# Kernel optimization log

Measured on AMD Instinct MI355X. Metric: run time of the kernel, lower is better.

Reference implementation:

```python
import jax, jax.numpy as jnp
import numpy as np

N_LAYERS = 2  # config['layer']
U_, L_, T_, A_ = 200000, 20000, 48, 2000
D_, D3_ = 96, 32
NNZ_ = 2_000_000


def _spmm(rows, cols, vals, x, n_rows):
    # y = A @ x for COO sparse A of shape [n_rows, n_cols]; x: [n_cols, d]
    return jax.ops.segment_sum(vals[:, None] * x[cols], rows, num_segments=n_rows)


def _attn_fuse(z, W1, b1, w2):
    # Attention module: project = Linear(d3,d3)+Tanh+Linear(d3,1, no bias)
    # z: [N, C, d3]; softmax over the C fused channels (dim=1)
    w = jnp.tanh(z @ W1 + b1) @ w2            # [N, C, 1]
    beta = jax.nn.softmax(w, axis=1)
    return jnp.sum(beta * z, axis=1)          # [N, d3]


def setup_inputs() -> dict:
    key = jax.random.key(0)
    ks = iter(jax.random.split(key, 64))
    inp = {}
    inp['user_emb'] = jax.random.normal(next(ks), (U_, D_), jnp.float32) * 0.1
    inp['loc_emb'] = jax.random.normal(next(ks), (L_, D3_), jnp.float32) * 0.1
    inp['time_emb'] = jax.random.normal(next(ks), (T_, D3_), jnp.float32) * 0.1
    inp['act_emb'] = jax.random.normal(next(ks), (A_, D3_), jnp.float32) * 0.1
    for f in ('l', 't', 'a'):
        s = 1.0 / np.sqrt(D3_)
        inp[f'W1_{f}'] = jax.random.normal(next(ks), (D3_, D3_), jnp.float32) * s
        inp[f'b1_{f}'] = jnp.zeros((D3_,), jnp.float32)
        inp[f'w2_{f}'] = jax.random.normal(next(ks), (D3_, 1), jnp.float32) * s

    def add_sparse(prefix, n_rows, n_cols):
        inp[prefix + '_rows'] = jax.random.randint(next(ks), (NNZ_,), 0, n_rows, jnp.int32)
        inp[prefix + '_cols'] = jax.random.randint(next(ks), (NNZ_,), 0, n_cols, jnp.int32)
        inp[prefix + '_vals'] = jax.random.uniform(next(ks), (NNZ_,), jnp.float32) * 0.01

    for p in ('normL', 'normT', 'normA', 'normLT', 'normLA', 'normTA', 'normLTA'):
        add_sparse(p, U_, U_)
    add_sparse('vtoeL', L_, U_)
    add_sparse('vtoeT', T_, U_)
    add_sparse('vtoeA', A_, U_)
    return inp


def reference(user_emb, loc_emb, time_emb, act_emb,
              W1_l, b1_l, w2_l, W1_t, b1_t, w2_t, W1_a, b1_a, w2_a,
              normL_rows, normL_cols, normL_vals,
              normT_rows, normT_cols, normT_vals,
              normA_rows, normA_cols, normA_vals,
              normLT_rows, normLT_cols, normLT_vals,
              normLA_rows, normLA_cols, normLA_vals,
              normTA_rows, normTA_cols, normTA_vals,
              normLTA_rows, normLTA_cols, normLTA_vals,
              vtoeL_rows, vtoeL_cols, vtoeL_vals,
              vtoeT_rows, vtoeT_cols, vtoeT_vals,
              vtoeA_rows, vtoeA_cols, vtoeA_vals):
    U = user_emb.shape[0]
    L, T, A = loc_emb.shape[0], time_emb.shape[0], act_emb.shape[0]
    # disentangle user embedding into 3 factor chunks (torch.split)
    u_l, u_t, u_a = jnp.split(user_emb, 3, axis=-1)
    u_l_all, u_t_all, u_a_all = [u_l], [u_t], [u_a]
    l_e, t_e, a_e = loc_emb, time_emb, act_emb
    l_all, t_all, a_all = [l_e], [t_e], [a_e]
    for _ in range(N_LAYERS):
        # intra-type hypergraph propagation per factor (4 hyperedge types each)
        zl = jnp.stack([
            _spmm(normL_rows, normL_cols, normL_vals, u_l, U),
            _spmm(normLT_rows, normLT_cols, normLT_vals, u_l, U),
            _spmm(normLA_rows, normLA_cols, normLA_vals, u_l, U),
            _spmm(normLTA_rows, normLTA_cols, normLTA_vals, u_l, U)], axis=1)
        zt = jnp.stack([
            _spmm(normT_rows, normT_cols, normT_vals, u_t, U),
            _spmm(normLT_rows, normLT_cols, normLT_vals, u_t, U),
            _spmm(normTA_rows, normTA_cols, normTA_vals, u_t, U),
            _spmm(normLTA_rows, normLTA_cols, normLTA_vals, u_t, U)], axis=1)
        za = jnp.stack([
            _spmm(normA_rows, normA_cols, normA_vals, u_a, U),
            _spmm(normLA_rows, normLA_cols, normLA_vals, u_a, U),
            _spmm(normTA_rows, normTA_cols, normTA_vals, u_a, U),
            _spmm(normLTA_rows, normLTA_cols, normLTA_vals, u_a, U)], axis=1)
        # hyperedge (location/time/activity) updates: vertex -> edge aggregation
        l_e = _spmm(vtoeL_rows, vtoeL_cols, vtoeL_vals, u_l, L)
        t_e = _spmm(vtoeT_rows, vtoeT_cols, vtoeT_vals, u_t, T)
        a_e = _spmm(vtoeA_rows, vtoeA_cols, vtoeA_vals, u_a, A)
        # inter-type attention fusion
        u_l = _attn_fuse(zl, W1_l, b1_l, w2_l)
        u_t = _attn_fuse(zt, W1_t, b1_t, w2_t)
        u_a = _attn_fuse(za, W1_a, b1_a, w2_a)
        u_l_all.append(u_l); u_t_all.append(u_t); u_a_all.append(u_a)
        l_all.append(l_e); t_all.append(t_e); a_all.append(a_e)
    mean = lambda xs: jnp.mean(jnp.stack(xs, 0), 0)
    users = jnp.concatenate([mean(u_l_all), mean(u_t_all), mean(u_a_all)], axis=-1)
    return users, mean(l_all), mean(t_all), mean(a_all)
```

## Files before the change

kernel.cpp:

```cpp
#include <hip/hip_runtime.h>
#include <cmath>

#define U_N 200000
#define L_N 20000
#define T_N 48
#define A_N 2000

#define VAL_SCALE_INV 9.5367431640625e-7f
#define BSHIFT 6
#define CAP_U 800
#define NBUCK_U 3125
#define CHUNK 8192
#define NSL_SH 3
#define NSL (1 << NSL_SH)
#define CAP_SL 40
#define NSA_SH 5
#define NSA (1 << NSA_SH)
#define CAP_SA 80
#define NST_SH 8
#define NST (1 << NST_SH)
#define CAP_ST 256
#define THIRD 0.33333333333333333f

__device__ __forceinline__ unsigned short f2bf(float f) {
    unsigned u = __float_as_uint(f);
    return (unsigned short)((u + 0x7FFFu + ((u >> 16) & 1u)) >> 16);
}
__device__ __forceinline__ float bf2f(unsigned short us) {
    return __uint_as_float(((unsigned)us) << 16);
}
__device__ __forceinline__ float blo(unsigned w) { return __uint_as_float(w << 16); }
__device__ __forceinline__ float bhi(unsigned w) { return __uint_as_float(w & 0xFFFF0000u); }
__device__ __forceinline__ float gfma(const unsigned short* __restrict__ x, unsigned e, int lane) {
    float xv = bf2f(x[((size_t)(e >> 14) << 5) + lane]);
    return xv * ((float)(e & 16383u) * VAL_SCALE_INV);
}
__device__ __forceinline__ unsigned quant14(float v) {
    unsigned q = (unsigned)(v * 1048576.0f + 0.5f);
    return q > 16383u ? 16383u : q;
}

__global__ void k_init_users(const float* __restrict__ ue,
                             unsigned short* __restrict__ u_l, unsigned short* __restrict__ u_t,
                             unsigned short* __restrict__ u_a, float* __restrict__ out_users) {
    int i = blockIdx.x * blockDim.x + threadIdx.x;
    if (i >= U_N * 96) return;
    float v = ue[i];
    out_users[i] = v * THIRD;
    int u = i / 96;
    int d = i - u * 96;
    unsigned short b = f2bf(v);
    if (d < 32)       u_l[u * 32 + d]      = b;
    else if (d < 64)  u_t[u * 32 + d - 32] = b;
    else              u_a[u * 32 + d - 64] = b;
}

__global__ void k_seed_edges(const float* __restrict__ le, const float* __restrict__ te,
                             const float* __restrict__ ae,
                             float* __restrict__ ol, float* __restrict__ ot,
                             float* __restrict__ oa) {
    int i = blockIdx.x * blockDim.x + threadIdx.x;
    int nl = L_N * 32, nt = T_N * 32, na = A_N * 32;
    if (i < nl) ol[i] = le[i] * THIRD;
    else if (i < nl + nt) ot[i - nl] = te[i - nl] * THIRD;
    else if (i < nl + nt + na) oa[i - nl - nt] = ae[i - nl - nt] * THIRD;
}

struct CurIni { int* p; int n; int cap; };
struct CurIni10 { CurIni s[10]; };

__global__ void k_cinit(CurIni10 B) {
    CurIni s = B.s[blockIdx.y];
    int i = blockIdx.x * blockDim.x + threadIdx.x;
    if (i < s.n) s.p[i] = i * s.cap;
}

struct USeg { const int* r; const int* c; const float* v; int nnz;
              int* bcur; unsigned long long* stage; };
struct UPass { USeg s[3]; int b0[3]; int n; };

__global__ void __launch_bounds__(256) k_passA_multi(UPass P) {
    int b = blockIdx.x;
    int m = 0;
    if (P.n > 1 && b >= P.b0[1]) m = 1;
    if (P.n > 2 && b >= P.b0[2]) m = 2;
    const USeg S = P.s[m];
    int base = (b - P.b0[m]) * CHUNK;
    int n = min(CHUNK, S.nnz - base);
    int t = threadIdx.x;

    __shared__ int cnt[NBUCK_U];
    __shared__ int cur[NBUCK_U];
    for (int i = t; i < NBUCK_U; i += 256) cnt[i] = 0;
    __syncthreads();
    for (int i = t; i < n; i += 256)
        atomicAdd(&cnt[S.r[base + i] >> BSHIFT], 1);
    __syncthreads();
    for (int bb = t; bb < NBUCK_U; bb += 256) {
        int c = cnt[bb];
        cur[bb] = c ? atomicAdd(&S.bcur[bb], c) : 0;
    }
    __syncthreads();
    for (int i = t; i < n; i += 256) {
        int r = S.r[base + i];
        int bkt = r >> BSHIFT;
        int p = atomicAdd(&cur[bkt], 1);
        if (p < (bkt + 1) * CAP_U)
            S.stage[p] = ((unsigned long long)(unsigned)r << 38) |
                         ((unsigned long long)(unsigned)S.c[base + i] << 14) |
                         quant14(S.v[base + i]);
    }
}

struct FSeg { const unsigned long long* stage; const int* bcur;
              int2* rp2; unsigned* pk; };
struct UFin { FSeg s[3]; };

__global__ void k_fin_multi(UFin F) {
    int m = blockIdx.x / NBUCK_U;
    int b = blockIdx.x - m * NBUCK_U;
    const FSeg S = F.s[m];
    int t = threadIdx.x;
    __shared__ int cnt[64];
    __shared__ int lscan[64];
    __shared__ int cur[64];
    __shared__ unsigned pkb[CAP_U];
    int beg = b * CAP_U;
    int end = min(S.bcur[b], beg + CAP_U);
    int n = end - beg;
    if (t < 64) cnt[t] = 0;
    __syncthreads();
    for (int e = beg + t; e < end; e += 256)
        atomicAdd(&cnt[(int)(S.stage[e] >> 38) & 63], 1);
    __syncthreads();
    if (t == 0) {
        int run = 0;
        for (int i = 0; i < 64; ++i) { lscan[i] = run; run += cnt[i]; }
    }
    __syncthreads();
    int r0 = b << BSHIFT;
    if (t < 64) {
        S.rp2[r0 + t] = make_int2(beg + lscan[t], beg + lscan[t] + cnt[t]);
        cur[t] = lscan[t];
    }
    __syncthreads();
    for (int e = beg + t; e < end; e += 256) {
        unsigned long long v = S.stage[e];
        int p = atomicAdd(&cur[(int)(v >> 38) & 63], 1);
        pkb[p] = (unsigned)v;
    }
    __syncthreads();
    for (int i = t; i < n; i += 256) S.pk[beg + i] = pkb[i];
}

struct VSeg { const int* r; const int* c; const float* v; int nnz;
              int nsshift; int nsmask; int cap; int* bcur; unsigned* gap; };
struct VPass { VSeg s[3]; int b0[3]; int n; };

__global__ void k_passV_multi(VPass P) {
    int b = blockIdx.x;
    int m = 0;
    if (P.n > 1 && b >= P.b0[1]) m = 1;
    if (P.n > 2 && b >= P.b0[2]) m = 2;
    const VSeg S = P.s[m];
    int i = (b - P.b0[m]) * 256 + threadIdx.x;
    if (i >= S.nnz) return;
    int slot = (S.r[i] << S.nsshift) | (i & S.nsmask);
    int p = atomicAdd(&S.bcur[slot], 1);
    if (p >= slot * S.cap + S.cap) return;
    S.gap[p] = ((unsigned)S.c[i] << 14) | quant14(S.v[i]);
}

__global__ void __launch_bounds__(256)
k_mega3(const int2* __restrict__ rp0, const unsigned* __restrict__ pk0,
        const int2* __restrict__ rp1, const unsigned* __restrict__ pk1,
        const int2* __restrict__ rp2, const unsigned* __restrict__ pk2,
        const int2* __restrict__ rp3, const unsigned* __restrict__ pk3,
        const unsigned short* __restrict__ x,
        const float* __restrict__ W1, const float* __restrict__ b1,
        const float* __restrict__ w2,
        unsigned short* __restrict__ u_out, float* __restrict__ out_users, int f) {
    __shared__ float sW[1024];
    __shared__ float sb[32];
    __shared__ float sw2[32];
    int t = threadIdx.x;
    for (int i = t; i < 1024; i += 256) sW[i] = W1[i];
    if (t < 32) { sb[t] = b1[t]; sw2[t] = w2[t]; }
    __syncthreads();

    int ch = t & 3;
    int u  = t >> 2;
    int r  = blockIdx.x * 64 + u;

    const int2* rp = (ch == 0) ? rp0 : (ch == 1) ? rp1 : (ch == 2) ? rp2 : rp3;
    const unsigned* pk = (ch == 0) ? pk0 : (ch == 1) ? pk1 : (ch == 2) ? pk2 : pk3;

    float acc[32];
#pragma unroll
    for (int d = 0; d < 32; ++d) acc[d] = 0.f;

    const int2 be = rp[r];
    int j = be.x, end = be.y;
    for (; j < end; j += 2) {
        unsigned e0 = pk[j];
        unsigned e1 = (j + 1 < end) ? pk[j + 1] : 0u;
        float v0 = (float)(e0 & 16383u) * VAL_SCALE_INV;
        float v1 = (j + 1 < end) ? (float)(e1 & 16383u) * VAL_SCALE_INV : 0.f;
        const uint4* xr0 = (const uint4*)(x + ((size_t)(e0 >> 14) << 5));
        const uint4* xr1 = (const uint4*)(x + ((size_t)(e1 >> 14) << 5));
        uint4 A0 = xr0[0], B0 = xr0[1], C0 = xr0[2], D0 = xr0[3];
        uint4 A1 = xr1[0], B1 = xr1[1], C1 = xr1[2], D1 = xr1[3];
#define UPD(wA, wB, base) \
        acc[base]     = fmaf(v0, blo(wA), acc[base]); \
        acc[base]     = fmaf(v1, blo(wB), acc[base]); \
        acc[base + 1] = fmaf(v0, bhi(wA), acc[base + 1]); \
        acc[base + 1] = fmaf(v1, bhi(wB), acc[base + 1]);
        UPD(A0.x, A1.x, 0)  UPD(A0.y, A1.y, 2)  UPD(A0.z, A1.z, 4)  UPD(A0.w, A1.w, 6)
        UPD(B0.x, B1.x, 8)  UPD(B0.y, B1.y, 10) UPD(B0.z, B1.z, 12) UPD(B0.w, B1.w, 14)
        UPD(C0.x, C1.x, 16) UPD(C0.y, C1.y, 18) UPD(C0.z, C1.z, 20) UPD(C0.w, C1.w, 22)
        UPD(D0.x, D1.x, 24) UPD(D0.y, D1.y, 26) UPD(D0.z, D1.z, 28) UPD(D0.w, D1.w, 30)
#undef UPD
    }

    float wsc = 0.f;
#pragma unroll 4
    for (int jj = 0; jj < 32; ++jj) {
        float h = sb[jj];
#pragma unroll
        for (int i = 0; i < 32; ++i) h = fmaf(acc[i], sW[i * 32 + jj], h);
        wsc = fmaf(tanhf(h), sw2[jj], wsc);
    }

    float m = fmaxf(wsc, __shfl_xor(wsc, 1, 4));
    m = fmaxf(m, __shfl_xor(m, 2, 4));
    float e = __expf(wsc - m);
    float s = e + __shfl_xor(e, 1, 4);
    s = s + __shfl_xor(s, 2, 4);
    float beta = e / s;

    float out8[8];
#pragma unroll
    for (int d = 0; d < 32; ++d) {
        float bz = beta * acc[d];
        bz += __shfl_xor(bz, 1, 4);
        bz += __shfl_xor(bz, 2, 4);
        if ((d >> 3) == ch) out8[d & 7] = bz;
    }

    unsigned p0 = (unsigned)f2bf(out8[0]) | ((unsigned)f2bf(out8[1]) << 16);
    unsigned p1 = (unsigned)f2bf(out8[2]) | ((unsigned)f2bf(out8[3]) << 16);
    unsigned p2 = (unsigned)f2bf(out8[4]) | ((unsigned)f2bf(out8[5]) << 16);
    unsigned p3 = (unsigned)f2bf(out8[6]) | ((unsigned)f2bf(out8[7]) << 16);
    *(uint4*)(u_out + (size_t)r * 32 + ch * 8) = make_uint4(p0, p1, p2, p3);

    float4* ou = (float4*)(out_users + (size_t)r * 96 + f * 32 + ch * 8);
    float4 a = ou[0];
    a.x += out8[0] * THIRD; a.y += out8[1] * THIRD;
    a.z += out8[2] * THIRD; a.w += out8[3] * THIRD;
    ou[0] = a;
    float4 b = ou[1];
    b.x += out8[4] * THIRD; b.y += out8[5] * THIRD;
    b.z += out8[6] * THIRD; b.w += out8[7] * THIRD;
    ou[1] = b;
}

__global__ void __launch_bounds__(256)
k_vtoe_sl(const int* __restrict__ bcur, const unsigned* __restrict__ gap,
          int CAP, int nsshift, const unsigned short* __restrict__ x,
          float* __restrict__ out, int n_slots) {
    int gid = (blockIdx.x * 256 + threadIdx.x) >> 5;
    int lane = threadIdx.x & 31;
    if (gid >= n_slots) return;
    int r = gid >> nsshift;
    int beg = gid * CAP;
    int end = min(bcur[gid], beg + CAP);
    if (beg >= end) return;
    float a = 0.f;
    int j = beg;
    for (; j + 4 <= end; j += 4) {
        unsigned t0 = gap[j], t1 = gap[j + 1], t2 = gap[j + 2], t3 = gap[j + 3];
        a += gfma(x, t0, lane); a += gfma(x, t1, lane);
        a += gfma(x, t2, lane); a += gfma(x, t3, lane);
    }
    for (; j < end; ++j) a += gfma(x, gap[j], lane);
    atomicAdd(&out[(size_t)r * 32 + lane], a * THIRD);
}

__global__ void k_init_users_f32(const float* __restrict__ ue,
                                 float* __restrict__ u_l, float* __restrict__ u_t,
                                 float* __restrict__ u_a, float* __restrict__ out_users) {
    int i = blockIdx.x * blockDim.x + threadIdx.x;
    if (i >= U_N * 96) return;
    float v = ue[i];
    out_users[i] = v;
    int u = i / 96;
    int d = i - u * 96;
    if (d < 32)       u_l[u * 32 + d]      = v;
    else if (d < 64)  u_t[u * 32 + d - 32] = v;
    else              u_a[u * 32 + d - 64] = v;
}

__global__ void k_spmm(const int* __restrict__ rows, const int* __restrict__ cols,
                       const float* __restrict__ vals, int nnz,
                       const float* __restrict__ x, float* __restrict__ y) {
    int tid = blockIdx.x * blockDim.x + threadIdx.x;
    int nz = tid >> 5;
    if (nz >= nnz) return;
    int d = tid & 31;
    atomicAdd(&y[(size_t)rows[nz] * 32 + d], vals[nz] * x[(size_t)cols[nz] * 32 + d]);
}

__global__ void k_spmm_smallT(const int* __restrict__ rows, const int* __restrict__ cols,
                              const float* __restrict__ vals, int nnz,
                              const float* __restrict__ x, float* __restrict__ y) {
    __shared__ float acc[T_N * 32];
    for (int i = threadIdx.x; i < T_N * 32; i += blockDim.x) acc[i] = 0.f;
    __syncthreads();
    int d = threadIdx.x & 31;
    int grp = threadIdx.x >> 5;
    int per_block = (nnz + gridDim.x - 1) / gridDim.x;
    int start = blockIdx.x * per_block;
    int end = min(nnz, start + per_block);
    for (int nz = start + grp; nz < end; nz += (blockDim.x >> 5))
        atomicAdd(&acc[rows[nz] * 32 + d], vals[nz] * x[(size_t)cols[nz] * 32 + d]);
    __syncthreads();
    for (int i = threadIdx.x; i < T_N * 32; i += blockDim.x)
        if (acc[i] != 0.f) atomicAdd(&y[i], acc[i]);
}

__global__ void k_attn(const float* __restrict__ z, const float* __restrict__ W1,
                       const float* __restrict__ b1, const float* __restrict__ w2,
                       float* __restrict__ u_out, float* __restrict__ out_users, int f) {
    __shared__ float sW[32 * 32];
    __shared__ float sb[32];
    __shared__ float sw2[32];
    for (int i = threadIdx.x; i < 1024; i += blockDim.x) sW[i] = W1[i];
    if (threadIdx.x < 32) { sb[threadIdx.x] = b1[threadIdx.x]; sw2[threadIdx.x] = w2[threadIdx.x]; }
    __syncthreads();
    int half = threadIdx.x >> 5;
    int j = threadIdx.x & 31;
    int u = blockIdx.x * 8 + half;
    if (u >= U_N) return;
    float zk[4];
#pragma unroll
    for (int k = 0; k < 4; ++k) zk[k] = z[(size_t)k * (U_N * 32) + (size_t)u * 32 + j];
    float w[4];
#pragma unroll
    for (int k = 0; k < 4; ++k) {
        float h = sb[j];
#pragma unroll
        for (int i = 0; i < 32; ++i) h += __shfl(zk[k], i, 32) * sW[i * 32 + j];
        float p = tanhf(h) * sw2[j];
#pragma unroll
        for (int off = 16; off; off >>= 1) p += __shfl_xor(p, off, 32);
        w[k] = p;
    }
    float m = fmaxf(fmaxf(w[0], w[1]), fmaxf(w[2], w[3]));
    float e0 = __expf(w[0] - m), e1 = __expf(w[1] - m), e2 = __expf(w[2] - m), e3 = __expf(w[3] - m);
    float inv = 1.f / (e0 + e1 + e2 + e3);
    float o = (e0 * zk[0] + e1 * zk[1] + e2 * zk[2] + e3 * zk[3]) * inv;
    u_out[(size_t)u * 32 + j] = o;
    out_users[(size_t)u * 96 + f * 32 + j] += o;
}

__global__ void k_scale(float* __restrict__ out, int n) {
    int i = blockIdx.x * blockDim.x + threadIdx.x;
    if (i < n) out[i] *= (1.0f / 3.0f);
}

extern "C" void kernel_launch(void* const* d_in, const int* in_sizes, int n_in,
                              void* d_out, int out_size, void* d_ws, size_t ws_size,
                              hipStream_t stream) {
    const float* user_emb = (const float*)d_in[0];
    const float* loc_emb  = (const float*)d_in[1];
    const float* time_emb = (const float*)d_in[2];
    const float* act_emb  = (const float*)d_in[3];
    const float* W1s[3] = {(const float*)d_in[4], (const float*)d_in[7], (const float*)d_in[10]};
    const float* b1s[3] = {(const float*)d_in[5], (const float*)d_in[8], (const float*)d_in[11]};
    const float* w2s[3] = {(const float*)d_in[6], (const float*)d_in[9], (const float*)d_in[12]};

    struct Mat { const int* r; const int* c; const float* v; int nnz; int nrows; };
    auto mk = [&](int base, int nrows) {
        return Mat{(const int*)d_in[base], (const int*)d_in[base + 1],
                   (const float*)d_in[base + 2], in_sizes[base], nrows};
    };
    Mat M[10] = {mk(13, U_N), mk(16, U_N), mk(19, U_N), mk(22, U_N), mk(25, U_N),
                 mk(28, U_N), mk(31, U_N), mk(34, L_N), mk(37, T_N), mk(40, A_N)};

    float* out       = (float*)d_out;
    float* out_users = out;
    float* out_l     = out + (size_t)U_N * 96;
    float* out_t     = out_l + (size_t)L_N * 32;
    float* out_a     = out_t + (size_t)T_N * 32;

    const int chmat[3][4] = {{0, 3, 4, 6}, {1, 3, 5, 6}, {2, 4, 5, 6}};

    auto align256 = [](size_t x) { return (x + 255) & ~(size_t)255; };
    char* wsb = (char*)d_ws;
    size_t off = 0;
    size_t ubuf_off[4];
    for (int b = 0; b < 4; ++b) { ubuf_off[b] = off; off = align256(off + (size_t)U_N * 32 * 2); }
    size_t rp2_off[7], pk_off[7], bcurU_off[7];
    for (int b = 0; b < 7; ++b) { rp2_off[b] = off; off = align256(off + (size_t)U_N * 8); }
    for (int b = 0; b < 7; ++b) { bcurU_off[b] = off; off = align256(off + (size_t)NBUCK_U * 4); }
    for (int b = 0; b < 7; ++b) { pk_off[b] = off; off = align256(off + (size_t)NBUCK_U * CAP_U * 4); }
    size_t bcurL_off = off; off = align256(off + (size_t)L_N * NSL * 4);
    size_t bcurA_off = off; off = align256(off + (size_t)A_N * NSA * 4);
    size_t bcurT_off = off; off = align256(off + (size_t)T_N * NST * 4);
    size_t gapA_bytes = (size_t)A_N * NSA * CAP_SA * 4;
    size_t gapT_bytes = (size_t)T_N * NST * CAP_ST * 4;
    size_t stage_bytes = (size_t)NBUCK_U * CAP_U * 8;
    size_t s2_bytes = align256(gapA_bytes) + align256(gapT_bytes);
    if (s2_bytes < stage_bytes) s2_bytes = stage_bytes;
    size_t s2_off = off; off = align256(off + s2_bytes);
    size_t gapL_bytes = (size_t)L_N * NSL * CAP_SL * 4;
    size_t s1_bytes = (stage_bytes > gapL_bytes) ? stage_bytes : gapL_bytes;
    size_t s1_off = off; off = align256(off + s1_bytes);
    size_t NEED = off;

    if (ws_size >= NEED) {
        unsigned long long* stg1 = (unsigned long long*)(wsb + s1_off);
        unsigned long long* stg2 = (unsigned long long*)(wsb + s2_off);
        unsigned long long* stg3 = (unsigned long long*)(wsb + pk_off[4]);
        int* bcurL = (int*)(wsb + bcurL_off);
        int* bcurA = (int*)(wsb + bcurA_off);
        int* bcurT = (int*)(wsb + bcurT_off);
        unsigned* gapL = (unsigned*)(wsb + s1_off);
        unsigned* gapA = (unsigned*)(wsb + s2_off);
        unsigned* gapT = (unsigned*)(wsb + s2_off + align256(gapA_bytes));

        CurIni10 B;
        for (int b = 0; b < 7; ++b)
            B.s[b] = CurIni{(int*)(wsb + bcurU_off[b]), NBUCK_U, CAP_U};
        B.s[7] = CurIni{bcurL, L_N * NSL, CAP_SL};
        B.s[8] = CurIni{bcurA, A_N * NSA, CAP_SA};
        B.s[9] = CurIni{bcurT, T_N * NST, CAP_ST};
        k_cinit<<<dim3((L_N * NSL + 255) / 256, 10), 256, 0, stream>>>(B);

        unsigned short* bufs[4];
        for (int b = 0; b < 4; ++b) bufs[b] = (unsigned short*)(wsb + ubuf_off[b]);
        k_init_users<<<(U_N * 96 + 255) / 256, 256, 0, stream>>>(
            user_emb, bufs[0], bufs[1], bufs[2], out_users);
        int nseed = (L_N + T_N + A_N) * 32;
        k_seed_edges<<<(nseed + 255) / 256, 256, 0, stream>>>(
            loc_emb, time_emb, act_emb, out_l, out_t, out_a);

        unsigned long long* stgs[3] = {stg1, stg2, stg3};
        auto runPhase = [&](const int* mats, int n) {
            UPass P; P.n = n;
            int blk = 0;
            for (int k = 0; k < n; ++k) {
                int m = mats[k];
                P.s[k] = USeg{M[m].r, M[m].c, M[m].v, M[m].nnz,
                              (int*)(wsb + bcurU_off[m]), stgs[k]};
                P.b0[k] = blk;
                blk += (M[m].nnz + CHUNK - 1) / CHUNK;
            }
            k_passA_multi<<<blk, 256, 0, stream>>>(P);
            UFin F;
            for (int k = 0; k < n; ++k) {
                int m = mats[k];
                F.s[k] = FSeg{stgs[k], (const int*)(wsb + bcurU_off[m]),
                              (int2*)(wsb + rp2_off[m]), (unsigned*)(wsb + pk_off[m])};
            }
            k_fin_multi<<<n * NBUCK_U, 256, 0, stream>>>(F);
        };
        const int ph1[3] = {0, 1, 2};
        const int ph2[2] = {3, 4};
        const int ph3[2] = {5, 6};
        runPhase(ph1, 3);
        runPhase(ph2, 2);
        runPhase(ph3, 2);

        {
            VPass P; P.n = 3;
            int blk = 0;
            VSeg segs[3] = {
                VSeg{M[7].r, M[7].c, M[7].v, M[7].nnz, NSL_SH, NSL - 1, CAP_SL, bcurL, gapL},
                VSeg{M[9].r, M[9].c, M[9].v, M[9].nnz, NSA_SH, NSA - 1, CAP_SA, bcurA, gapA},
                VSeg{M[8].r, M[8].c, M[8].v, M[8].nnz, NST_SH, NST - 1, CAP_ST, bcurT, gapT}};
            for (int k = 0; k < 3; ++k) {
                P.s[k] = segs[k];
                P.b0[k] = blk;
                blk += (segs[k].nnz + 255) / 256;
            }
            k_passV_multi<<<blk, 256, 0, stream>>>(P);
        }

        unsigned short* ucur[3] = {bufs[0], bufs[1], bufs[2]};
        unsigned short* uspare = bufs[3];
        auto rpP = [&](int b) { return (const int2*)(wsb + rp2_off[b]); };
        auto pkP = [&](int b) { return (const unsigned*)(wsb + pk_off[b]); };

        for (int f = 0; f < 3; ++f) {
            const int* cm = chmat[f];
            for (int layer = 0; layer < 2; ++layer) {
                if (f == 0)
                    k_vtoe_sl<<<((size_t)L_N * NSL * 32 + 255) / 256, 256, 0, stream>>>(
                        bcurL, gapL, CAP_SL, NSL_SH, ucur[0], out_l, L_N * NSL);
                else if (f == 1)
                    k_vtoe_sl<<<((size_t)T_N * NST * 32 + 255) / 256, 256, 0, stream>>>(
                        bcurT, gapT, CAP_ST, NST_SH, ucur[1], out_t, T_N * NST);
                else
                    k_vtoe_sl<<<((size_t)A_N * NSA * 32 + 255) / 256, 256, 0, stream>>>(
                        bcurA, gapA, CAP_SA, NSA_SH, ucur[2], out_a, A_N * NSA);
                k_mega3<<<NBUCK_U, 256, 0, stream>>>(
                    rpP(cm[0]), pkP(cm[0]), rpP(cm[1]), pkP(cm[1]),
                    rpP(cm[2]), pkP(cm[2]), rpP(cm[3]), pkP(cm[3]),
                    ucur[f], W1s[f], b1s[f], w2s[f], uspare, out_users, f);
                unsigned short* t = ucur[f]; ucur[f] = uspare; uspare = t;
            }
        }
    } else {
        float* ws = (float*)d_ws;
        float* z = ws;
        float* u[3];
        u[0] = ws + (size_t)4 * U_N * 32;
        u[1] = u[0] + (size_t)U_N * 32;
        u[2] = u[1] + (size_t)U_N * 32;
        k_init_users_f32<<<(U_N * 96 + 255) / 256, 256, 0, stream>>>(
            user_emb, u[0], u[1], u[2], out_users);
        hipMemcpyAsync(out_l, loc_emb,  (size_t)L_N * 32 * 4, hipMemcpyDeviceToDevice, stream);
        hipMemcpyAsync(out_t, time_emb, (size_t)T_N * 32 * 4, hipMemcpyDeviceToDevice, stream);
        hipMemcpyAsync(out_a, act_emb,  (size_t)A_N * 32 * 4, hipMemcpyDeviceToDevice, stream);
        float* oute[3] = {out_l, out_t, out_a};
        for (int layer = 0; layer < 2; ++layer) {
            for (int f = 0; f < 3; ++f) {
                hipMemsetAsync(z, 0, (size_t)4 * U_N * 32 * 4, stream);
                for (int k = 0; k < 4; ++k) {
                    Mat& m = M[chmat[f][k]];
                    k_spmm<<<((size_t)m.nnz * 32 + 255) / 256, 256, 0, stream>>>(
                        m.r, m.c, m.v, m.nnz, u[f], z + (size_t)k * U_N * 32);
                }
                Mat& vm = M[7 + f];
                if (f == 1)
                    k_spmm_smallT<<<2048, 256, 0, stream>>>(vm.r, vm.c, vm.v, vm.nnz, u[f], oute[f]);
                else
                    k_spmm<<<((size_t)vm.nnz * 32 + 255) / 256, 256, 0, stream>>>(
                        vm.r, vm.c, vm.v, vm.nnz, u[f], oute[f]);
                k_attn<<<(U_N + 7) / 8, 256, 0, stream>>>(z, W1s[f], b1s[f], w2s[f], u[f], out_users, f);
            }
        }
        int total = U_N * 96 + L_N * 32 + T_N * 32 + A_N * 32;
        k_scale<<<(total + 255) / 256, 256, 0, stream>>>(out, total);
    }
}
```

Baseline: 2.095 ms.

## Build compact per-row CSR for vertex-to-edge matrices instead of sliced slot buffers

Replaces the per-nonzero atomic scatter into fixed-capacity slices (rows × slices × cap) for the location, activity and time vertex-to-edge matrices with block-local counting sorts. Location goes through a bucket-plus-finalize path that yields a compact CSR. Activity and time rows use one contiguous per-row region filled by a shared-memory histogram pass. The aggregation kernels now split each row's contiguous range across S warps. The aim is fewer global atomics during build, smaller and denser gather buffers, and better locality on the x lookups. The fixed per-row capacities (CAP_LB, CAP_AR, CAP_TR) can drop entries if a row overflows, and the build adds an extra finalize launch.

New measurement: 2.140 ms. +2.2%, slower.

```diff
diff --git a/kernel.cpp b/kernel.cpp
--- a/kernel.cpp
+++ b/kernel.cpp
@@ -7,19 +7,18 @@
 #define A_N 2000
 
 #define VAL_SCALE_INV 9.5367431640625e-7f
-#define BSHIFT 6
+#define CHUNK 8192
+#define BSHIFT_U 6
+#define NBUCK_U 3125
 #define CAP_U 800
-#define NBUCK_U 3125
-#define CHUNK 8192
-#define NSL_SH 3
-#define NSL (1 << NSL_SH)
-#define CAP_SL 40
-#define NSA_SH 5
-#define NSA (1 << NSA_SH)
-#define CAP_SA 80
-#define NST_SH 8
-#define NST (1 << NST_SH)
-#define CAP_ST 256
+#define BSHIFT_L 3
+#define NBUCK_L 2500
+#define CAP_LB 1088
+#define CAP_AR 1280
+#define CAP_TR 44032
+#define SL_C 4
+#define SA_C 32
+#define ST_C 1024
 #define THIRD 0.33333333333333333f
 
 __device__ __forceinline__ unsigned short f2bf(float f) {
@@ -76,6 +75,7 @@
 }
 
 struct USeg { const int* r; const int* c; const float* v; int nnz;
+              int bshift; int nbuck; int cap;
               int* bcur; unsigned long long* stage; };
 struct UPass { USeg s[3]; int b0[3]; int n; };
 
@@ -91,21 +91,21 @@
 
     __shared__ int cnt[NBUCK_U];
     __shared__ int cur[NBUCK_U];
-    for (int i = t; i < NBUCK_U; i += 256) cnt[i] = 0;
+    for (int i = t; i < S.nbuck; i += 256) cnt[i] = 0;
     __syncthreads();
     for (int i = t; i < n; i += 256)
-        atomicAdd(&cnt[S.r[base + i] >> BSHIFT], 1);
-    __syncthreads();
-    for (int bb = t; bb < NBUCK_U; bb += 256) {
+        atomicAdd(&cnt[S.r[base + i] >> S.bshift], 1);
+    __syncthreads();
+    for (int bb = t; bb < S.nbuck; bb += 256) {
         int c = cnt[bb];
         cur[bb] = c ? atomicAdd(&S.bcur[bb], c) : 0;
     }
     __syncthreads();
     for (int i = t; i < n; i += 256) {
         int r = S.r[base + i];
-        int bkt = r >> BSHIFT;
+        int bkt = r >> S.bshift;
         int p = atomicAdd(&cur[bkt], 1);
-        if (p < (bkt + 1) * CAP_U)
+        if (p < (bkt + 1) * S.cap)
             S.stage[p] = ((unsigned long long)(unsigned)r << 38) |
                          ((unsigned long long)(unsigned)S.c[base + i] << 14) |
                          quant14(S.v[base + i]);
@@ -113,62 +113,82 @@
 }
 
 struct FSeg { const unsigned long long* stage; const int* bcur;
-              int2* rp2; unsigned* pk; };
-struct UFin { FSeg s[3]; };
+              int2* rp2; unsigned* pk; int bshift; int cap; };
+struct UFin { FSeg s[3]; int b0[3]; int n; };
 
 __global__ void k_fin_multi(UFin F) {
-    int m = blockIdx.x / NBUCK_U;
-    int b = blockIdx.x - m * NBUCK_U;
+    int b = blockIdx.x;
+    int m = 0;
+    if (F.n > 1 && b >= F.b0[1]) m = 1;
+    if (F.n > 2 && b >= F.b0[2]) m = 2;
     const FSeg S = F.s[m];
+    b -= F.b0[m];
     int t = threadIdx.x;
+    int rpb = 1 << S.bshift;
+    int rmask = rpb - 1;
     __shared__ int cnt[64];
     __shared__ int lscan[64];
     __shared__ int cur[64];
-    __shared__ unsigned pkb[CAP_U];
-    int beg = b * CAP_U;
-    int end = min(S.bcur[b], beg + CAP_U);
+    __shared__ unsigned pkb[1152];
+    int beg = b * S.cap;
+    int end = min(S.bcur[b], beg + S.cap);
     int n = end - beg;
-    if (t < 64) cnt[t] = 0;
+    if (t < rpb) cnt[t] = 0;
     __syncthreads();
     for (int e = beg + t; e < end; e += 256)
-        atomicAdd(&cnt[(int)(S.stage[e] >> 38) & 63], 1);
+        atomicAdd(&cnt[(int)(S.stage[e] >> 38) & rmask], 1);
     __syncthreads();
     if (t == 0) {
         int run = 0;
-        for (int i = 0; i < 64; ++i) { lscan[i] = run; run += cnt[i]; }
-    }
-    __syncthreads();
-    int r0 = b << BSHIFT;
-    if (t < 64) {
-        S.rp2[r0 + t] = make_int2(beg + lscan[t], beg + lscan[t] + cnt[t]);
+        for (int i = 0; i < rpb; ++i) { lscan[i] = run; run += cnt[i]; }
+    }
+    __syncthreads();
+    int r0 = b << S.bshift;
+    if (t < rpb) {
+        int s0 = min(lscan[t], S.cap);
+        int s1 = min(lscan[t] + cnt[t], S.cap);
+        S.rp2[r0 + t] = make_int2(beg + s0, beg + s1);
         cur[t] = lscan[t];
     }
     __syncthreads();
     for (int e = beg + t; e < end; e += 256) {
         unsigned long long v = S.stage[e];
-        int p = atomicAdd(&cur[(int)(v >> 38) & 63], 1);
+        int p = atomicAdd(&cur[(int)(v >> 38) & rmask], 1);
         pkb[p] = (unsigned)v;
     }
     __syncthreads();
     for (int i = t; i < n; i += 256) S.pk[beg + i] = pkb[i];
 }
 
-struct VSeg { const int* r; const int* c; const float* v; int nnz;
-              int nsshift; int nsmask; int cap; int* bcur; unsigned* gap; };
-struct VPass { VSeg s[3]; int b0[3]; int n; };
-
-__global__ void k_passV_multi(VPass P) {
+struct RSeg { const int* r; const int* c; const float* v; int nnz;
+              int nrow; int cap; int* bcur; unsigned* gap; };
+struct RPass { RSeg s[2]; int b0[2]; int n; };
+
+__global__ void __launch_bounds__(256) k_passR_multi(RPass P) {
     int b = blockIdx.x;
     int m = 0;
     if (P.n > 1 && b >= P.b0[1]) m = 1;
-    if (P.n > 2 && b >= P.b0[2]) m = 2;
-    const VSeg S = P.s[m];
-    int i = (b - P.b0[m]) * 256 + threadIdx.x;
-    if (i >= S.nnz) return;
-    int slot = (S.r[i] << S.nsshift) | (i & S.nsmask);
-    int p = atomicAdd(&S.bcur[slot], 1);
-    if (p >= slot * S.cap + S.cap) return;
-    S.gap[p] = ((unsigned)S.c[i] << 14) | quant14(S.v[i]);
+    const RSeg S = P.s[m];
+    int base = (b - P.b0[m]) * CHUNK;
+    int n = min(CHUNK, S.nnz - base);
+    int t = threadIdx.x;
+    __shared__ int cnt[2048];
+    for (int i = t; i < S.nrow; i += 256) cnt[i] = 0;
+    __syncthreads();
+    for (int i = t; i < n; i += 256)
+        atomicAdd(&cnt[S.r[base + i]], 1);
+    __syncthreads();
+    for (int rr = t; rr < S.nrow; rr += 256) {
+        int c = cnt[rr];
+        cnt[rr] = c ? atomicAdd(&S.bcur[rr], c) : 0;
+    }
+    __syncthreads();
+    for (int i = t; i < n; i += 256) {
+        int r = S.r[base + i];
+        int p = atomicAdd(&cnt[r], 1);
+        if (p < (r + 1) * S.cap)
+            S.gap[p] = ((unsigned)S.c[base + i] << 14) | quant14(S.v[base + i]);
+    }
 }
 
 __global__ void __launch_bounds__(256)
@@ -265,24 +285,53 @@
 }
 
 __global__ void __launch_bounds__(256)
-k_vtoe_sl(const int* __restrict__ bcur, const unsigned* __restrict__ gap,
-          int CAP, int nsshift, const unsigned short* __restrict__ x,
-          float* __restrict__ out, int n_slots) {
+k_vtoe_rp(const int2* __restrict__ rp2, const unsigned* __restrict__ pk,
+          const unsigned short* __restrict__ x, float* __restrict__ out,
+          int n_rows, int S) {
     int gid = (blockIdx.x * 256 + threadIdx.x) >> 5;
     int lane = threadIdx.x & 31;
-    if (gid >= n_slots) return;
-    int r = gid >> nsshift;
-    int beg = gid * CAP;
-    int end = min(bcur[gid], beg + CAP);
-    if (beg >= end) return;
+    if (gid >= n_rows * S) return;
+    int r = gid / S, s = gid - r * S;
+    int2 be = rp2[r];
+    int len = be.y - be.x;
+    int chunk = (len + S - 1) / S;
+    int b = be.x + s * chunk;
+    int e = min(be.y, b + chunk);
+    if (b >= e) return;
     float a = 0.f;
-    int j = beg;
-    for (; j + 4 <= end; j += 4) {
+    int j = b;
+    for (; j + 4 <= e; j += 4) {
+        unsigned t0 = pk[j], t1 = pk[j + 1], t2 = pk[j + 2], t3 = pk[j + 3];
+        a += gfma(x, t0, lane); a += gfma(x, t1, lane);
+        a += gfma(x, t2, lane); a += gfma(x, t3, lane);
+    }
+    for (; j < e; ++j) a += gfma(x, pk[j], lane);
+    atomicAdd(&out[(size_t)r * 32 + lane], a * THIRD);
+}
+
+__global__ void __launch_bounds__(256)
+k_vtoe_gap(const int* __restrict__ bcur, const unsigned* __restrict__ gap,
+           int CAP, const unsigned short* __restrict__ x,
+           float* __restrict__ out, int n_rows, int S) {
+    int gid = (blockIdx.x * 256 + threadIdx.x) >> 5;
+    int lane = threadIdx.x & 31;
+    if (gid >= n_rows * S) return;
+    int r = gid / S, s = gid - r * S;
+    int beg = r * CAP;
+    int end = min(bcur[r], beg + CAP);
+    int len = end - beg;
+    int chunk = (len + S - 1) / S;
+    int b = beg + s * chunk;
+    int e = min(end, b + chunk);
+    if (b >= e) return;
+    float a = 0.f;
+    int j = b;
+    for (; j + 4 <= e; j += 4) {
         unsigned t0 = gap[j], t1 = gap[j + 1], t2 = gap[j + 2], t3 = gap[j + 3];
         a += gfma(x, t0, lane); a += gfma(x, t1, lane);
         a += gfma(x, t2, lane); a += gfma(x, t3, lane);
     }
-    for (; j < end; ++j) a += gfma(x, gap[j], lane);
+    for (; j < e; ++j) a += gfma(x, gap[j], lane);
     atomicAdd(&out[(size_t)r * 32 + lane], a * THIRD);
 }
 
@@ -404,17 +453,19 @@
     for (int b = 0; b < 7; ++b) { rp2_off[b] = off; off = align256(off + (size_t)U_N * 8); }
     for (int b = 0; b < 7; ++b) { bcurU_off[b] = off; off = align256(off + (size_t)NBUCK_U * 4); }
     for (int b = 0; b < 7; ++b) { pk_off[b] = off; off = align256(off + (size_t)NBUCK_U * CAP_U * 4); }
-    size_t bcurL_off = off; off = align256(off + (size_t)L_N * NSL * 4);
-    size_t bcurA_off = off; off = align256(off + (size_t)A_N * NSA * 4);
-    size_t bcurT_off = off; off = align256(off + (size_t)T_N * NST * 4);
-    size_t gapA_bytes = (size_t)A_N * NSA * CAP_SA * 4;
-    size_t gapT_bytes = (size_t)T_N * NST * CAP_ST * 4;
-    size_t stage_bytes = (size_t)NBUCK_U * CAP_U * 8;
+    size_t rp2L_off = off; off = align256(off + (size_t)L_N * 8);
+    size_t bcurL_off = off; off = align256(off + (size_t)NBUCK_L * 4);
+    size_t pkL_off  = off; off = align256(off + (size_t)NBUCK_L * CAP_LB * 4);
+    size_t bcurA_off = off; off = align256(off + (size_t)A_N * 4);
+    size_t bcurT_off = off; off = align256(off + (size_t)T_N * 4);
+    size_t gapA_bytes = (size_t)A_N * CAP_AR * 4;
+    size_t gapT_bytes = (size_t)T_N * CAP_TR * 4;
+    size_t stageU_bytes = (size_t)NBUCK_U * CAP_U * 8;
     size_t s2_bytes = align256(gapA_bytes) + align256(gapT_bytes);
-    if (s2_bytes < stage_bytes) s2_bytes = stage_bytes;
+    if (s2_bytes < stageU_bytes) s2_bytes = stageU_bytes;
     size_t s2_off = off; off = align256(off + s2_bytes);
-    size_t gapL_bytes = (size_t)L_N * NSL * CAP_SL * 4;
-    size_t s1_bytes = (stage_bytes > gapL_bytes) ? stage_bytes : gapL_bytes;
+    size_t stageL_bytes = (size_t)NBUCK_L * CAP_LB * 8;
+    size_t s1_bytes = (stageU_bytes > stageL_bytes) ? stageU_bytes : stageL_bytes;
     size_t s1_off = off; off = align256(off + s1_bytes);
     size_t NEED = off;
 
@@ -425,17 +476,16 @@
         int* bcurL = (int*)(wsb + bcurL_off);
         int* bcurA = (int*)(wsb + bcurA_off);
         int* bcurT = (int*)(wsb + bcurT_off);
-        unsigned* gapL = (unsigned*)(wsb + s1_off);
         unsigned* gapA = (unsigned*)(wsb + s2_off);
         unsigned* gapT = (unsigned*)(wsb + s2_off + align256(gapA_bytes));
 
         CurIni10 B;
         for (int b = 0; b < 7; ++b)
             B.s[b] = CurIni{(int*)(wsb + bcurU_off[b]), NBUCK_U, CAP_U};
-        B.s[7] = CurIni{bcurL, L_N * NSL, CAP_SL};
-        B.s[8] = CurIni{bcurA, A_N * NSA, CAP_SA};
-        B.s[9] = CurIni{bcurT, T_N * NST, CAP_ST};
-        k_cinit<<<dim3((L_N * NSL + 255) / 256, 10), 256, 0, stream>>>(B);
+        B.s[7] = CurIni{bcurL, NBUCK_L, CAP_LB};
+        B.s[8] = CurIni{bcurA, A_N, CAP_AR};
+        B.s[9] = CurIni{bcurT, T_N, CAP_TR};
+        k_cinit<<<dim3((NBUCK_U + 255) / 256, 10), 256, 0, stream>>>(B);
 
         unsigned short* bufs[4];
         for (int b = 0; b < 4; ++b) bufs[b] = (unsigned short*)(wsb + ubuf_off[b]);
@@ -452,16 +502,19 @@
             for (int k = 0; k < n; ++k) {
                 int m = mats[k];
                 P.s[k] = USeg{M[m].r, M[m].c, M[m].v, M[m].nnz,
+                              BSHIFT_U, NBUCK_U, CAP_U,
                               (int*)(wsb + bcurU_off[m]), stgs[k]};
                 P.b0[k] = blk;
                 blk += (M[m].nnz + CHUNK - 1) / CHUNK;
             }
             k_passA_multi<<<blk, 256, 0, stream>>>(P);
-            UFin F;
+            UFin F; F.n = n;
             for (int k = 0; k < n; ++k) {
                 int m = mats[k];
                 F.s[k] = FSeg{stgs[k], (const int*)(wsb + bcurU_off[m]),
-                              (int2*)(wsb + rp2_off[m]), (unsigned*)(wsb + pk_off[m])};
+                              (int2*)(wsb + rp2_off[m]), (unsigned*)(wsb + pk_off[m]),
+                              BSHIFT_U, CAP_U};
+                F.b0[k] = k * NBUCK_U;
             }
             k_fin_multi<<<n * NBUCK_U, 256, 0, stream>>>(F);
         };
@@ -473,18 +526,27 @@
         runPhase(ph3, 2);
 
         {
-            VPass P; P.n = 3;
-            int blk = 0;
-            VSeg segs[3] = {
-                VSeg{M[7].r, M[7].c, M[7].v, M[7].nnz, NSL_SH, NSL - 1, CAP_SL, bcurL, gapL},
-                VSeg{M[9].r, M[9].c, M[9].v, M[9].nnz, NSA_SH, NSA - 1, CAP_SA, bcurA, gapA},
-                VSeg{M[8].r, M[8].c, M[8].v, M[8].nnz, NST_SH, NST - 1, CAP_ST, bcurT, gapT}};
-            for (int k = 0; k < 3; ++k) {
-                P.s[k] = segs[k];
-                P.b0[k] = blk;
-                blk += (segs[k].nnz + 255) / 256;
-            }
-            k_passV_multi<<<blk, 256, 0, stream>>>(P);
+            UPass P; P.n = 1;
+            P.s[0] = USeg{M[7].r, M[7].c, M[7].v, M[7].nnz,
+                          BSHIFT_L, NBUCK_L, CAP_LB, bcurL, stg1};
+            P.b0[0] = 0;
+            k_passA_multi<<<(M[7].nnz + CHUNK - 1) / CHUNK, 256, 0, stream>>>(P);
+            UFin F; F.n = 1;
+            F.s[0] = FSeg{stg1, bcurL, (int2*)(wsb + rp2L_off),
+                          (unsigned*)(wsb + pkL_off), BSHIFT_L, CAP_LB};
+            F.b0[0] = 0;
+            k_fin_multi<<<NBUCK_L, 256, 0, stream>>>(F);
+        }
+
+        {
+            RPass P; P.n = 2;
+            P.s[0] = RSeg{M[9].r, M[9].c, M[9].v, M[9].nnz, A_N, CAP_AR, bcurA, gapA};
+            P.b0[0] = 0;
+            int blk = (M[9].nnz + CHUNK - 1) / CHUNK;
+            P.s[1] = RSeg{M[8].r, M[8].c, M[8].v, M[8].nnz, T_N, CAP_TR, bcurT, gapT};
+            P.b0[1] = blk;
+            blk += (M[8].nnz + CHUNK - 1) / CHUNK;
+            k_passR_multi<<<blk, 256, 0, stream>>>(P);
         }
 
         unsigned short* ucur[3] = {bufs[0], bufs[1], bufs[2]};
@@ -496,14 +558,15 @@
             const int* cm = chmat[f];
             for (int layer = 0; layer < 2; ++layer) {
                 if (f == 0)
-                    k_vtoe_sl<<<((size_t)L_N * NSL * 32 + 255) / 256, 256, 0, stream>>>(
-                        bcurL, gapL, CAP_SL, NSL_SH, ucur[0], out_l, L_N * NSL);
+                    k_vtoe_rp<<<((size_t)L_N * SL_C * 32 + 255) / 256, 256, 0, stream>>>(
+                        (const int2*)(wsb + rp2L_off), (const unsigned*)(wsb + pkL_off),
+                        ucur[0], out_l, L_N, SL_C);
                 else if (f == 1)
-                    k_vtoe_sl<<<((size_t)T_N * NST * 32 + 255) / 256, 256, 0, stream>>>(
-                        bcurT, gapT, CAP_ST, NST_SH, ucur[1], out_t, T_N * NST);
+                    k_vtoe_gap<<<((size_t)T_N * ST_C * 32 + 255) / 256, 256, 0, stream>>>(
+                        bcurT, gapT, CAP_TR, ucur[1], out_t, T_N, ST_C);
                 else
-                    k_vtoe_sl<<<((size_t)A_N * NSA * 32 + 255) / 256, 256, 0, stream>>>(
-                        bcurA, gapA, CAP_SA, NSA_SH, ucur[2], out_a, A_N * NSA);
+                    k_vtoe_gap<<<((size_t)A_N * SA_C * 32 + 255) / 256, 256, 0, stream>>>(
+                        bcurA, gapA, CAP_AR, ucur[2], out_a, A_N, SA_C);
                 k_mega3<<<NBUCK_U, 256, 0, stream>>>(
                     rpP(cm[0]), pkP(cm[0]), rpP(cm[1]), pkP(cm[1]),
                     rpP(cm[2]), pkP(cm[2]), rpP(cm[3]), pkP(cm[3]),
```
